# Performance work log

Hardware: AMD Instinct MI355X
Metric: run time of the kernel (lower is better)

Reference implementation:

```python
import jax, jax.numpy as jnp
import numpy as np

N = 10000   # nodes
E = 100000  # edges
B = 64      # graphs
HID = 128


def setup_inputs() -> dict:
    key = jax.random.key(0)
    ks = iter(jax.random.split(key, 64))
    def nrm(shape, s=0.1):
        return jax.random.normal(next(ks), shape, dtype=jnp.float32) * s
    inp = {}
    inp["x"] = nrm((N, 1), 1.0)
    inp["node_type"] = jax.random.randint(next(ks), (N,), 0, 2)
    inp["edge_index"] = jax.random.randint(next(ks), (2, E), 0, N)
    inp["edge_attr"] = nrm((E, 1), 1.0)
    inp["batch"] = jnp.sort(jax.random.randint(next(ks), (N,), 0, B))
    inp["vp_w"] = nrm((1, HID)); inp["vp_b"] = nrm((HID,))
    inp["type_emb"] = nrm((2, HID))
    def conv(pre, fin, h, c):
        inp[pre + "_wl"] = nrm((fin, h * c)); inp[pre + "_bl"] = nrm((h * c,))
        inp[pre + "_wr"] = nrm((fin, h * c)); inp[pre + "_br"] = nrm((h * c,))
        inp[pre + "_we"] = nrm((1, h * c));  inp[pre + "_att"] = nrm((h, c))
        inp[pre + "_bias"] = nrm((h * c if pre != "c3" else c,))
    conv("c1", HID, 8, HID)
    conv("c2", HID * 8, 2, HID)
    conv("c3", HID * 2, 1, HID)
    inp["m1_w"] = nrm((HID, HID)); inp["m1_b"] = nrm((HID,))
    inp["ln1_g"] = jnp.ones((HID,), jnp.float32); inp["ln1_b"] = jnp.zeros((HID,), jnp.float32)
    inp["m2_w"] = nrm((HID, HID // 2)); inp["m2_b"] = nrm((HID // 2,))
    inp["ln2_g"] = jnp.ones((HID // 2,), jnp.float32); inp["ln2_b"] = jnp.zeros((HID // 2,), jnp.float32)
    inp["m3_w"] = nrm((HID // 2, 1)); inp["m3_b"] = nrm((1,))
    return inp


def _gatv2(x, src, dst, ea, wl, bl, wr, br, we, att, bias, heads, out_ch, concat):
    """PyG GATv2Conv (eval mode): add self-loops (edge_attr fill='mean' over dst),
    attn = (att * leaky_relu(Wl x_src + Wr x_dst + We e)).sum(-1), segment-softmax
    over destination, scatter-add of alpha * Wl x_src."""
    n = x.shape[0]
    ones = jnp.ones((ea.shape[0], 1), ea.dtype)
    deg = jax.ops.segment_sum(ones, dst, num_segments=n)
    loop_attr = jax.ops.segment_sum(ea, dst, num_segments=n) / jnp.maximum(deg, 1.0)
    ar = jnp.arange(n, dtype=src.dtype)
    src2 = jnp.concatenate([src, ar])
    dst2 = jnp.concatenate([dst, ar])
    ea2 = jnp.concatenate([ea, loop_attr], axis=0)
    xl = (x @ wl + bl).reshape(n, heads, out_ch)   # source transform
    xr = (x @ wr + br).reshape(n, heads, out_ch)   # target transform
    e = (ea2 @ we).reshape(-1, heads, out_ch)      # [E2, H, C]
    msg = xl[src2]                                 # [E2, H, C]
    z = jax.nn.leaky_relu(msg + xr[dst2] + e, 0.2)
    score = jnp.einsum('ehc,hc->eh', z, att)       # [E2, H]
    smax = jax.ops.segment_max(score, dst2, num_segments=n)
    ex = jnp.exp(score - smax[dst2])
    denom = jax.ops.segment_sum(ex, dst2, num_segments=n)
    alpha = ex / denom[dst2]
    out = jax.ops.segment_sum(alpha[:, :, None] * msg, dst2, num_segments=n)
    out = out.reshape(n, heads * out_ch) if concat else out.mean(axis=1)
    return out + bias


def _layernorm(v, g, b):
    mu = v.mean(-1, keepdims=True)
    var = v.var(-1, keepdims=True)
    return (v - mu) / jnp.sqrt(var + 1e-5) * g + b


def reference(x, node_type, edge_index, edge_attr, batch,
              vp_w, vp_b, type_emb,
              c1_wl, c1_bl, c1_wr, c1_br, c1_we, c1_att, c1_bias,
              c2_wl, c2_bl, c2_wr, c2_br, c2_we, c2_att, c2_bias,
              c3_wl, c3_bl, c3_wr, c3_br, c3_we, c3_att, c3_bias,
              m1_w, m1_b, ln1_g, ln1_b, m2_w, m2_b, ln2_g, ln2_b, m3_w, m3_b):
    src, dst = edge_index[0], edge_index[1]
    h = x @ vp_w + vp_b + type_emb[node_type]
    h = jax.nn.leaky_relu(_gatv2(h, src, dst, edge_attr, c1_wl, c1_bl, c1_wr, c1_br, c1_we, c1_att, c1_bias, 8, HID, True), 0.2)
    h = jax.nn.leaky_relu(_gatv2(h, src, dst, edge_attr, c2_wl, c2_bl, c2_wr, c2_br, c2_we, c2_att, c2_bias, 2, HID, True), 0.2)
    h = jax.nn.leaky_relu(_gatv2(h, src, dst, edge_attr, c3_wl, c3_bl, c3_wr, c3_br, c3_we, c3_att, c3_bias, 1, HID, False), 0.2)
    # masked global mean pool over node_type == 0
    w = (node_type == 0).astype(h.dtype)
    sums = jax.ops.segment_sum(h * w[:, None], batch, num_segments=B)
    cnts = jax.ops.segment_sum(w, batch, num_segments=B)
    pooled = sums / jnp.maximum(cnts, 1.0)[:, None]
    h1 = jax.nn.leaky_relu(_layernorm(pooled @ m1_w + m1_b, ln1_g, ln1_b), 0.2)
    h2 = jax.nn.leaky_relu(_layernorm(h1 @ m2_w + m2_b, ln2_g, ln2_b), 0.2)
    return (h2 @ m3_w + m3_b).squeeze(-1)
```

## Files before the change

kernel.cpp:

```cpp
#include <hip/hip_runtime.h>
#include <math.h>

#define NN 10000
#define NE 100000
#define E2 (NE + NN)
#define NBATCH 64

typedef short bf16x8 __attribute__((ext_vector_type(8)));
typedef float f32x4 __attribute__((ext_vector_type(4)));

__device__ __forceinline__ float lrelu(float v){ return v > 0.f ? v : 0.2f*v; }

__device__ __forceinline__ unsigned short f2bf(float x){
  unsigned int u = __float_as_uint(x);
  u += 0x7fffu + ((u >> 16) & 1u);
  return (unsigned short)(u >> 16);
}
__device__ __forceinline__ float bf2f(unsigned short u){
  return __uint_as_float(((unsigned int)u) << 16);
}

__global__ __launch_bounds__(256) void prep_kernel(
    const float* __restrict__ vp_w, const float* __restrict__ vp_b,
    const float* __restrict__ type_emb,
    const float* __restrict__ c1_wl, const float* __restrict__ c1_bl,
    const float* __restrict__ c1_wr, const float* __restrict__ c1_br,
    float* __restrict__ Ul, float* __restrict__ CTl,
    float* __restrict__ Ur, float* __restrict__ CT2,
    const float* __restrict__ c2_wl, const float* __restrict__ c2_wr,
    const float* __restrict__ c3_wl, const float* __restrict__ c3_wr,
    unsigned short* __restrict__ W2lT, unsigned short* __restrict__ W2rT,
    unsigned short* __restrict__ W3lT, unsigned short* __restrict__ W3rT,
    float* __restrict__ zbase, int zero_words)
{
  __shared__ float t[64][65];
  int b = blockIdx.x;
  int tid = threadIdx.x;
  if (b < 144){
    const float* in; unsigned short* out; int K, N, idx;
    if (b < 64)      { in=c2_wl; out=W2lT; K=1024; N=256; idx=b; }
    else if (b <128) { in=c2_wr; out=W2rT; K=1024; N=256; idx=b-64; }
    else if (b <136) { in=c3_wl; out=W3lT; K=256;  N=128; idx=b-128; }
    else             { in=c3_wr; out=W3rT; K=256;  N=128; idx=b-136; }
    int K64 = K >> 6;
    int kx = idx % K64, nx = idx / K64;
    int k0 = kx*64, n0 = nx*64;
    int lr = tid >> 4;
    int lc = (tid & 15) * 4;
#pragma unroll
    for (int i=0;i<4;++i){
      int r = lr + i*16;
      float4 v = *(const float4*)(in + (size_t)(k0+r)*N + n0 + lc);
      t[r][lc+0]=v.x; t[r][lc+1]=v.y; t[r][lc+2]=v.z; t[r][lc+3]=v.w;
    }
    __syncthreads();
    int sr = tid >> 3;
    int sc = (tid & 7) * 8;
#pragma unroll
    for (int i=0;i<2;++i){
      int n = sr + i*32;
      unsigned short tmp[8];
#pragma unroll
      for (int j=0;j<8;++j) tmp[j] = f2bf(t[sc+j][n]);
      unsigned short* op = out + (size_t)(n0+n)*K + k0 + sc;
      *(ushort4*)op       = make_ushort4(tmp[0],tmp[1],tmp[2],tmp[3]);
      *(ushort4*)(op + 4) = make_ushort4(tmp[4],tmp[5],tmp[6],tmp[7]);
    }
  } else if (b < 148){
    int j = (b-144)*256 + tid;
    float ul=0.f, c0l=0.f, c1l=0.f, ur=0.f, c0r=0.f, c1r=0.f;
    for (int k=0; k<128; ++k){
      float a = c1_wl[k*1024 + j], bb = c1_wr[k*1024 + j];
      float vw = vp_w[k], vb = vp_b[k], t0 = type_emb[k], t1 = type_emb[128+k];
      ul += vw*a; ur += vw*bb;
      c0l += (vb+t0)*a; c1l += (vb+t1)*a;
      c0r += (vb+t0)*bb; c1r += (vb+t1)*bb;
    }
    float bl = c1_bl[j], br = c1_br[j];
    Ul[j]=ul; Ur[j]=ur;
    CTl[j]      = c0l + bl;
    CTl[1024+j] = c1l + bl;
    CT2[j]        = (c0l+bl) + (c0r+br);
    CT2[1024+j]   = (c0l+bl) + (c1r+br);
    CT2[2048+j]   = (c1l+bl) + (c0r+br);
    CT2[3072+j]   = (c1l+bl) + (c1r+br);
  } else {
    for (int i = (b-148)*256 + tid; i < zero_words; i += 32*256)
      zbase[i] = 0.f;
  }
}

__global__ void count_kernel(const int* __restrict__ dst, const float* __restrict__ ea,
                             int* __restrict__ deg, float* __restrict__ loop_sum){
  int e = blockIdx.x*256 + threadIdx.x;
  if (e < NE){
    int d = dst[e];
    atomicAdd(&deg[d], 1);
    atomicAdd(&loop_sum[d], ea[e]);
  }
}

__global__ __launch_bounds__(1024) void scan_kernel(const int* __restrict__ deg,
    const float* __restrict__ loop_sum, int* __restrict__ rowptr, float* __restrict__ loop_attr){
  __shared__ int wsum[16];
  __shared__ int carry_s;
  int tid = threadIdx.x;
  int lane = tid & 63, wid = tid >> 6;
  if (tid == 0) carry_s = 0;
  __syncthreads();
  for (int base = 0; base < NN; base += 1024){
    int i = base + tid;
    int v = (i < NN) ? deg[i] : 0;
    int incl = v;
#pragma unroll
    for (int off = 1; off < 64; off <<= 1){
      int t = __shfl_up(incl, off, 64);
      if (lane >= off) incl += t;
    }
    if (lane == 63) wsum[wid] = incl;
    __syncthreads();
    int pre = carry_s;
    for (int w = 0; w < wid; ++w) pre += wsum[w];
    if (i < NN){
      rowptr[i] = pre + incl - v;
      loop_attr[i] = loop_sum[i] / fmaxf((float)v, 1.f);
    }
    __syncthreads();
    if (tid == 0){
      int t = 0;
      for (int w = 0; w < 16; ++w) t += wsum[w];
      carry_s += t;
    }
    __syncthreads();
  }
  if (tid == 0) rowptr[NN] = carry_s;
}

__global__ void fill_kernel(const int* __restrict__ src, const int* __restrict__ dst,
                            const float* __restrict__ ea, const int* __restrict__ rowptr,
                            int* __restrict__ rowctr, int* __restrict__ srcs,
                            int* __restrict__ dsts, float* __restrict__ eav){
  int e = blockIdx.x*256 + threadIdx.x;
  if (e < NE){
    int d = dst[e];
    int p = rowptr[d] + atomicAdd(&rowctr[d], 1);
    srcs[p] = src[e];
    dsts[p] = d;
    eav[p] = ea[e];
  }
}

__global__ __launch_bounds__(256) void conv1_score(
    const int* __restrict__ srcs, const int* __restrict__ dsts, const float* __restrict__ eav,
    const float* __restrict__ loop_attr, const float* __restrict__ x, const int* __restrict__ ntype,
    const float* __restrict__ Ul, const float* __restrict__ Ur, const float* __restrict__ CT2,
    const float* __restrict__ we, const float* __restrict__ att,
    float* __restrict__ scores)
{
  __shared__ float ldsct[4096];
  int tid = threadIdx.x;
  for (int i = tid; i < 1024; i += 256)
    *(float4*)&ldsct[i*4] = *(const float4*)&CT2[i*4];
  int te = tid & 127;
  int sub = tid >> 7;
  int ch0 = te * 8;
  float ul[8], ur[8], wev[8], atv[8];
#pragma unroll
  for (int v=0; v<8; ++v){
    ul[v]=Ul[ch0+v]; ur[v]=Ur[ch0+v]; wev[v]=we[ch0+v]; atv[v]=att[ch0+v];
  }
  __syncthreads();
  for (int j = blockIdx.x*2 + sub; j < E2; j += gridDim.x*2){
    int s, d; float ea;
    if (j < NE){ s = srcs[j]; d = dsts[j]; ea = eav[j]; }
    else       { s = j - NE;  d = s;       ea = loop_attr[s]; }
    float xs = x[s], xn = x[d];
    int tt = ntype[s]*2 + ntype[d];
    const float* cp = &ldsct[tt*1024 + ch0];
    float4 c0 = *(const float4*)cp;
    float4 c1 = *(const float4*)(cp+4);
    float ct[8] = {c0.x,c0.y,c0.z,c0.w,c1.x,c1.y,c1.z,c1.w};
    float p = 0.f;
#pragma unroll
    for (int v=0; v<8; ++v){
      float z = fmaf(xs, ul[v], fmaf(xn, ur[v], fmaf(ea, wev[v], ct[v])));
      p += atv[v]*lrelu(z);
    }
#pragma unroll
    for (int mm=1; mm<16; mm<<=1) p += __shfl_xor(p, mm, 16);
    if ((te & 15) == 0) scores[(size_t)j*8 + (te>>4)] = p;
  }
}

__global__ __launch_bounds__(256) void conv1_agg(
    const int* __restrict__ rowptr, const int* __restrict__ srcs,
    const float* __restrict__ scores, const float* __restrict__ x, const int* __restrict__ ntype,
    const float* __restrict__ Ul, const float* __restrict__ CTl,
    const float* __restrict__ bias, unsigned short* __restrict__ out)
{
  int n = blockIdx.x;
  int tid = threadIdx.x;
  int h = tid >> 5, el = tid & 31;
  int beg = rowptr[n], deg = rowptr[n+1] - beg;
  int cnt = deg + 1;
  float m = -1e30f, l = 0.f, s1 = 0.f, s20 = 0.f;
  for (int i = el; i < cnt; i += 32){
    int pos; int s;
    if (i < deg){ pos = beg + i; s = srcs[pos]; }
    else        { pos = NE + n;  s = n; }
    float p = scores[(size_t)pos*8 + h];
    float xs = x[s];
    float w0 = (ntype[s] == 0) ? 1.f : 0.f;
    float mn = fmaxf(m, p), f = __expf(m-mn), pe = __expf(p-mn);
    l = l*f + pe; s1 = s1*f + pe*xs; s20 = s20*f + pe*w0; m = mn;
  }
#pragma unroll
  for (int off=1; off<32; off<<=1){
    float mb = __shfl_xor(m, off, 32), lb = __shfl_xor(l, off, 32);
    float s1b = __shfl_xor(s1, off, 32), s20b = __shfl_xor(s20, off, 32);
    float mn = fmaxf(m, mb), fa = __expf(m-mn), fb = __expf(mb-mn);
    l = l*fa + lb*fb; s1 = s1*fa + s1b*fb; s20 = s20*fa + s20b*fb; m = mn;
  }
  float inv = 1.f/l;
  s1 *= inv; s20 *= inv;
  float s21 = 1.f - s20;
  int ch0 = tid * 4;
  float4 u  = *(const float4*)(Ul + ch0);
  float4 t0 = *(const float4*)(CTl + ch0);
  float4 t1 = *(const float4*)(CTl + 1024 + ch0);
  float4 bi = *(const float4*)(bias + ch0);
  ushort4 o;
  o.x = f2bf(lrelu(s1*u.x + s20*t0.x + s21*t1.x + bi.x));
  o.y = f2bf(lrelu(s1*u.y + s20*t0.y + s21*t1.y + bi.y));
  o.z = f2bf(lrelu(s1*u.z + s20*t0.z + s21*t1.z + bi.z));
  o.w = f2bf(lrelu(s1*u.w + s20*t0.w + s21*t1.w + bi.w));
  *(ushort4*)(out + (size_t)n*1024 + ch0) = o;
}

template<int H, int THREADS, int VPT, bool ONLY0, bool OUTBF, bool INBF>
__global__ __launch_bounds__(THREADS) void conv_kernel(
    const int* __restrict__ rowptr, const int* __restrict__ srcs, const float* __restrict__ eav,
    const float* __restrict__ loop_attr, const int* __restrict__ ntype,
    const void* __restrict__ Xv, int stride, int xr_off,
    const float* __restrict__ we, const float* __restrict__ att, const float* __restrict__ bias,
    void* __restrict__ out)
{
  const int HC = THREADS*VPT;
  const int TPH = THREADS/H;
  int n = blockIdx.x;
  if (ONLY0 && ntype[n] != 0) return;
  int tid = threadIdx.x;
  int ch0 = tid * VPT;
  const float* Xf = (const float*)Xv;
  const unsigned short* Xb = (const unsigned short*)Xv;
  float wev[VPT], atv[VPT], biv[VPT], xrv[VPT];
#pragma unroll
  for (int v=0; v<VPT; ++v){
    int ch = ch0+v;
    wev[v]=we[ch]; atv[v]=att[ch]; biv[v]=bias[ch];
  }
  if constexpr (INBF){
    ushort4 q = *(const ushort4*)(Xb + (size_t)n*stride + xr_off + ch0);
    xrv[0]=bf2f(q.x); xrv[1]=bf2f(q.y); xrv[2]=bf2f(q.z); xrv[3]=bf2f(q.w);
  } else {
#pragma unroll
    for (int v=0; v<VPT; ++v) xrv[v]=Xf[(size_t)n*stride + xr_off + ch0+v];
  }
  float ms[4], ls[4], A[4][VPT];
#pragma unroll
  for (int k=0; k<4; ++k){
    ms[k] = -INFINITY; ls[k] = 0.f;
#pragma unroll
    for (int v=0; v<VPT; ++v) A[k][v] = 0.f;
  }
  int beg=rowptr[n], end=rowptr[n+1];
  float la = loop_attr[n];
  for (int j=beg; j<=end; j+=4){
    bool val[4]; int sx[4]; float ex[4];
#pragma unroll
    for (int k=0; k<4; ++k){
      int pos = j + k;
      val[k] = pos <= end;
      sx[k] = (!val[k] || pos == end) ? n : srcs[pos];
      ex[k] = !val[k] ? 0.f : (pos == end ? la : eav[pos]);
    }
    float xv[4][VPT];
#pragma unroll
    for (int k=0; k<4; ++k){
      if constexpr (INBF){
        ushort4 q = *(const ushort4*)(Xb + (size_t)sx[k]*stride + ch0);
        xv[k][0]=bf2f(q.x); xv[k][1]=bf2f(q.y); xv[k][2]=bf2f(q.z); xv[k][3]=bf2f(q.w);
      } else if constexpr (VPT == 4){
        float4 q = *(const float4*)(Xf + (size_t)sx[k]*stride + ch0);
        xv[k][0]=q.x; xv[k][1]=q.y; xv[k][2]=q.z; xv[k][3]=q.w;
      } else {
        float2 q = *(const float2*)(Xf + (size_t)sx[k]*stride + ch0);
        xv[k][0]=q.x; xv[k][1]=q.y;
      }
    }
    float p[4];
#pragma unroll
    for (int k=0; k<4; ++k){
      float acc = 0.f;
#pragma unroll
      for (int v=0; v<VPT; ++v)
        acc += atv[v]*lrelu(xv[k][v]+xrv[v]+ex[k]*wev[v]);
      p[k] = acc;
    }
#pragma unroll
    for (int mm=1; mm<TPH; mm<<=1){
#pragma unroll
      for (int k=0; k<4; ++k) p[k] += __shfl_xor(p[k], mm, 64);
    }
#pragma unroll
    for (int k=0; k<4; ++k){
      if (val[k]){
        float mn=fmaxf(ms[k],p[k]), sc=__expf(ms[k]-mn), pe=__expf(p[k]-mn);
        ls[k]=ls[k]*sc+pe; ms[k]=mn;
#pragma unroll
        for (int v=0; v<VPT; ++v) A[k][v]=A[k][v]*sc+pe*xv[k][v];
      }
    }
  }
#pragma unroll
  for (int k=1; k<4; ++k){
    float mn = fmaxf(ms[0], ms[k]);
    float fa = __expf(ms[0]-mn), fb = __expf(ms[k]-mn);
    ls[0] = ls[0]*fa + ls[k]*fb;
#pragma unroll
    for (int v=0; v<VPT; ++v) A[0][v] = A[0][v]*fa + A[k][v]*fb;
    ms[0] = mn;
  }
  float inv = 1.f/ls[0];
  size_t baseo=(size_t)n*HC+ch0;
  if constexpr (OUTBF){
    unsigned short* ob = (unsigned short*)out;
    ushort4 o;
    o.x = f2bf(lrelu(A[0][0]*inv+biv[0]));
    o.y = f2bf(lrelu(A[0][1]*inv+biv[1]));
    o.z = f2bf(lrelu(A[0][2]*inv+biv[2]));
    o.w = f2bf(lrelu(A[0][3]*inv+biv[3]));
    *(ushort4*)(ob + baseo) = o;
  } else {
    float* of = (float*)out;
#pragma unroll
    for (int v=0; v<VPT; ++v) of[baseo+v]=lrelu(A[0][v]*inv+biv[v]);
  }
}

template<bool OUTBF>
__global__ __launch_bounds__(256) void gemm_dual_lds(
    const short* __restrict__ Abf,
    const short* __restrict__ WlT, const short* __restrict__ WrT,
    const float* __restrict__ bl, const float* __restrict__ br,
    void* __restrict__ Out, int M, int K, int NcH, int cgrid, int rgrid)
{
  __shared__ short lds[12288];
  int id = blockIdx.x;
  int xcd = id & 7, slot = id >> 3;
  int nb = slot % cgrid;
  int rowgroup = (slot / cgrid) * 8 + xcd;
  if (rowgroup >= rgrid) return;
  int row0 = rowgroup * 128;
  int NC2 = 2*NcH;
  int halfx = NcH >> 6;
  int isR = nb >= halfx;
  const short* WT = isR ? WrT : WlT;
  const float* bias = isR ? br : bl;
  int col0 = (nb - (isR ? halfx : 0)) * 64;
  int gcol0 = nb * 64;
  int tid = threadIdx.x;
  int lane = tid & 63, wave = tid >> 6;
  int wm = wave >> 1, wn = wave & 1;
  int quad = lane >> 4, l16 = lane & 15;

  const short* asrc[4];
#pragma unroll
  for (int i=0;i<4;++i){
    int c = wave*256 + i*64 + lane;
    int m = c >> 3, j = c & 7;
    int gr = row0 + m; gr = gr < M ? gr : M-1;
    asrc[i] = Abf + (size_t)gr*K + ((j ^ (m & 7)) << 3);
  }
  const short* bsrc[2];
#pragma unroll
  for (int i=0;i<2;++i){
    int c = wave*128 + i*64 + lane;
    int nloc = c >> 3, j = c & 7;
    bsrc[i] = WT + (size_t)(col0 + nloc)*K + ((j ^ (nloc & 7)) << 3);
  }

  float biasv[2] = { bias[col0 + wn*32 + l16], bias[col0 + wn*32 + 16 + l16] };
  f32x4 acc[4][2];
#pragma unroll
  for (int f=0; f<4; ++f)
#pragma unroll
    for (int g=0; g<2; ++g) acc[f][g] = (f32x4){0.f,0.f,0.f,0.f};

  int niter = K >> 6;
  for (int it=0; it<niter; ++it){
    int k0 = it << 6;
#pragma unroll
    for (int i=0;i<4;++i)
      __builtin_amdgcn_global_load_lds(asrc[i] + k0, &lds[(wave*256 + i*64)*8], 16, 0, 0);
#pragma unroll
    for (int i=0;i<2;++i)
      __builtin_amdgcn_global_load_lds(bsrc[i] + k0, &lds[8192 + (wave*128 + i*64)*8], 16, 0, 0);
    __syncthreads();
#pragma unroll
    for (int s=0; s<2; ++s){
      int t = s*4 + quad;
      bf16x8 af[4], bfv[2];
#pragma unroll
      for (int f=0; f<4; ++f){
        int m = wm*64 + f*16 + l16;
        af[f] = *(const bf16x8*)&lds[m*64 + ((t ^ (m & 7)) << 3)];
      }
#pragma unroll
      for (int g=0; g<2; ++g){
        int nloc = wn*32 + g*16 + l16;
        bfv[g] = *(const bf16x8*)&lds[8192 + nloc*64 + ((t ^ (nloc & 7)) << 3)];
      }
#pragma unroll
      for (int f=0; f<4; ++f)
#pragma unroll
        for (int g=0; g<2; ++g)
          acc[f][g] = __builtin_amdgcn_mfma_f32_16x16x32_bf16(af[f], bfv[g], acc[f][g], 0,0,0);
    }
    __syncthreads();
  }

#pragma unroll
  for (int f=0; f<4; ++f){
    int rbase = row0 + wm*64 + f*16 + quad*4;
#pragma unroll
    for (int r=0; r<4; ++r){
      int rr = rbase + r;
      if (rr < M){
#pragma unroll
        for (int g=0; g<2; ++g){
          int cc = gcol0 + wn*32 + g*16 + l16;
          float val = acc[f][g][r] + biasv[g];
          if constexpr (OUTBF) ((unsigned short*)Out)[(size_t)rr*NC2 + cc] = f2bf(val);
          else                 ((float*)Out)[(size_t)rr*NC2 + cc] = val;
        }
      }
    }
  }
}

__device__ __forceinline__ int lbound(const int* __restrict__ a, int n, int key){
  int lo = 0, hi = n;
  while (lo < hi){ int mid = (lo+hi) >> 1; if (a[mid] < key) lo = mid+1; else hi = mid; }
  return lo;
}

__global__ __launch_bounds__(128) void head_kernel(
    const float* __restrict__ h3, const int* __restrict__ ntype, const int* __restrict__ batch,
    const float* __restrict__ m1w, const float* __restrict__ m1b,
    const float* __restrict__ g1, const float* __restrict__ b1,
    const float* __restrict__ m2w, const float* __restrict__ m2b,
    const float* __restrict__ g2, const float* __restrict__ b2,
    const float* __restrict__ m3w, const float* __restrict__ m3b,
    float* __restrict__ out)
{
  __shared__ float p[128];
  __shared__ float hb[128];
  __shared__ float red[128];
  int b = blockIdx.x, j = threadIdx.x;
  int lo = lbound(batch, NN, b);
  int hi = lbound(batch, NN, b+1);
  float s = 0.f, cnt = 0.f;
  int n = lo;
  for (; n + 3 < hi; n += 4){
    float w0 = (ntype[n]   == 0) ? 1.f : 0.f;
    float w1 = (ntype[n+1] == 0) ? 1.f : 0.f;
    float w2 = (ntype[n+2] == 0) ? 1.f : 0.f;
    float w3 = (ntype[n+3] == 0) ? 1.f : 0.f;
    s += w0*h3[(size_t)n*128 + j]     + w1*h3[(size_t)(n+1)*128 + j]
       + w2*h3[(size_t)(n+2)*128 + j] + w3*h3[(size_t)(n+3)*128 + j];
    cnt += w0 + w1 + w2 + w3;
  }
  for (; n < hi; ++n){
    float w = (ntype[n] == 0) ? 1.f : 0.f;
    s += w*h3[(size_t)n*128 + j];
    cnt += w;
  }
  p[j] = s / fmaxf(cnt, 1.f);
  __syncthreads();
  float a = m1b[j];
  for (int k=0; k<128; ++k) a += p[k]*m1w[k*128 + j];
  red[j] = a; __syncthreads();
  for (int off=64; off>0; off>>=1){ if (j<off) red[j] += red[j+off]; __syncthreads(); }
  float mu = red[0] * (1.f/128.f);
  __syncthreads();
  float d = a - mu;
  red[j] = d*d; __syncthreads();
  for (int off=64; off>0; off>>=1){ if (j<off) red[j] += red[j+off]; __syncthreads(); }
  float var = red[0] * (1.f/128.f);
  __syncthreads();
  hb[j] = lrelu(d * rsqrtf(var + 1e-5f) * g1[j] + b1[j]);
  __syncthreads();
  float a2 = 0.f;
  if (j < 64){
    a2 = m2b[j];
    for (int k=0; k<128; ++k) a2 += hb[k]*m2w[k*64 + j];
  }
  red[j] = (j<64) ? a2 : 0.f; __syncthreads();
  for (int off=64; off>0; off>>=1){ if (j<off) red[j] += red[j+off]; __syncthreads(); }
  float mu2 = red[0] * (1.f/64.f);
  __syncthreads();
  float d2 = a2 - mu2;
  red[j] = (j<64) ? d2*d2 : 0.f; __syncthreads();
  for (int off=64; off>0; off>>=1){ if (j<off) red[j] += red[j+off]; __syncthreads(); }
  float var2 = red[0] * (1.f/64.f);
  __syncthreads();
  if (j < 64) hb[j] = lrelu(d2 * rsqrtf(var2 + 1e-5f) * g2[j] + b2[j]);
  __syncthreads();
  if (j == 0){
    float o = m3b[0];
    for (int k=0; k<64; ++k) o += hb[k]*m3w[k];
    out[b] = o;
  }
}

extern "C" void kernel_launch(void* const* d_in, const int* in_sizes, int n_in,
                              void* d_out, int out_size, void* d_ws, size_t ws_size,
                              hipStream_t stream)
{
  const float* x        = (const float*)d_in[0];
  const int*   ntype    = (const int*)d_in[1];
  const int*   ei       = (const int*)d_in[2];
  const float* eattr    = (const float*)d_in[3];
  const int*   batch    = (const int*)d_in[4];
  const float* vp_w     = (const float*)d_in[5];
  const float* vp_b     = (const float*)d_in[6];
  const float* type_emb = (const float*)d_in[7];
  const float* c1_wl = (const float*)d_in[8];  const float* c1_bl = (const float*)d_in[9];
  const float* c1_wr = (const float*)d_in[10]; const float* c1_br = (const float*)d_in[11];
  const float* c1_we = (const float*)d_in[12]; const float* c1_att= (const float*)d_in[13];
  const float* c1_bias=(const float*)d_in[14];
  const float* c2_wl = (const float*)d_in[15]; const float* c2_bl = (const float*)d_in[16];
  const float* c2_wr = (const float*)d_in[17]; const float* c2_br = (const float*)d_in[18];
  const float* c2_we = (const float*)d_in[19]; const float* c2_att= (const float*)d_in[20];
  const float* c2_bias=(const float*)d_in[21];
  const float* c3_wl = (const float*)d_in[22]; const float* c3_bl = (const float*)d_in[23];
  const float* c3_wr = (const float*)d_in[24]; const float* c3_br = (const float*)d_in[25];
  const float* c3_we = (const float*)d_in[26]; const float* c3_att= (const float*)d_in[27];
  const float* c3_bias=(const float*)d_in[28];
  const float* m1_w = (const float*)d_in[29]; const float* m1_b = (const float*)d_in[30];
  const float* ln1_g= (const float*)d_in[31]; const float* ln1_b= (const float*)d_in[32];
  const float* m2_w = (const float*)d_in[33]; const float* m2_b = (const float*)d_in[34];
  const float* ln2_g= (const float*)d_in[35]; const float* ln2_b= (const float*)d_in[36];
  const float* m3_w = (const float*)d_in[37]; const float* m3_b = (const float*)d_in[38];
  const int* esrc = ei;
  const int* edst = ei + NE;
  float* outp = (float*)d_out;
  (void)in_sizes; (void)n_in; (void)out_size; (void)ws_size;

  char* w = (char*)d_ws;
  auto alloc = [&](size_t bytes) -> void* {
    void* p = (void*)w;
    w += (bytes + 255) & ~(size_t)255;
    return p;
  };
  unsigned short* h1bf = (unsigned short*)alloc((size_t)NN*1024*2);
  unsigned short* X2   = (unsigned short*)alloc((size_t)NN*512*2);
  unsigned short* h2bf = (unsigned short*)alloc((size_t)NN*256*2);
  float* X3   = (float*)alloc((size_t)NN*256*4);
  float* h3   = (float*)alloc((size_t)NN*128*4);
  unsigned short* W2lT = (unsigned short*)alloc((size_t)256*1024*2);
  unsigned short* W2rT = (unsigned short*)alloc((size_t)256*1024*2);
  unsigned short* W3lT = (unsigned short*)alloc((size_t)128*256*2);
  unsigned short* W3rT = (unsigned short*)alloc((size_t)128*256*2);
  float* Ul   = (float*)alloc(1024*4);
  float* CTl  = (float*)alloc(2048*4);
  float* Ur   = (float*)alloc(1024*4);
  float* CT2  = (float*)alloc(4096*4);
  float* scores = (float*)alloc((size_t)E2*8*4);
  const int zero_words = 3*NN;
  float* zbase = (float*)alloc((size_t)zero_words*4);
  int*   deg      = (int*)zbase;
  int*   rowctr   = (int*)(zbase + NN);
  float* loop_sum = zbase + 2*NN;
  float* loop_attr= (float*)alloc((size_t)NN*4);
  int*   rowptr   = (int*)alloc((size_t)(NN+1)*4);
  int*   srcs     = (int*)alloc((size_t)NE*4);
  int*   dsts     = (int*)alloc((size_t)NE*4);
  float* eav      = (float*)alloc((size_t)NE*4);

  prep_kernel<<<180, 256, 0, stream>>>(vp_w, vp_b, type_emb,
      c1_wl, c1_bl, c1_wr, c1_br, Ul, CTl, Ur, CT2,
      c2_wl, c2_wr, c3_wl, c3_wr, W2lT, W2rT, W3lT, W3rT,
      zbase, zero_words);
  count_kernel<<<(NE+255)/256, 256, 0, stream>>>(edst, eattr, deg, loop_sum);
  scan_kernel<<<1, 1024, 0, stream>>>(deg, loop_sum, rowptr, loop_attr);
  fill_kernel<<<(NE+255)/256, 256, 0, stream>>>(esrc, edst, eattr, rowptr, rowctr,
                                                srcs, dsts, eav);
  conv1_score<<<2048, 256, 0, stream>>>(srcs, dsts, eav, loop_attr, x, ntype,
      Ul, Ur, CT2, c1_we, c1_att, scores);
  conv1_agg<<<NN, 256, 0, stream>>>(rowptr, srcs, scores, x, ntype,
      Ul, CTl, c1_bias, h1bf);
  gemm_dual_lds<true><<<640, 256, 0, stream>>>(
      (const short*)h1bf, (const short*)W2lT, (const short*)W2rT, c2_bl, c2_br,
      (void*)X2, NN, 1024, 256, 8, 79);
  conv_kernel<2,64,4,false,true,true><<<NN, 64, 0, stream>>>(rowptr, srcs, eav, loop_attr, ntype,
      (const void*)X2, 512, 256, c2_we, c2_att, c2_bias, h2bf);
  gemm_dual_lds<false><<<320, 256, 0, stream>>>(
      (const short*)h2bf, (const short*)W3lT, (const short*)W3rT, c3_bl, c3_br,
      (void*)X3, NN, 256, 128, 4, 79);
  conv_kernel<1,64,2,true,false,false><<<NN, 64, 0, stream>>>(rowptr, srcs, eav, loop_attr, ntype,
      (const void*)X3, 256, 128, c3_we, c3_att, c3_bias, h3);
  head_kernel<<<NBATCH, 128, 0, stream>>>(h3, ntype, batch, m1_w, m1_b, ln1_g, ln1_b,
                                          m2_w, m2_b, ln2_g, ln2_b, m3_w, m3_b, outp);
}
```

Before: 315.4 us.

## Prefetch next edge in conv1_score, swizzle LDS table, append self-loops to edge arrays

conv1_score now software-pipelines its grid-stride loop, loading the next edge's indices, features and type ahead of computing the current one. The per-type channel table in LDS is XOR-swizzled to cut bank conflicts on the float4 reads. Self-loop entries are written into the extended srcs/dsts/eav arrays during the scan, which removes the branch in the score loop. leaky_relu becomes a branchless fmax form and the accumulation uses fma. The cost is extra registers for the prefetched values and a few more stores in the single-block scan.

New measurement: 318.0 us. About the same (+0.8%).

```diff
diff --git a/kernel.cpp b/kernel.cpp
--- a/kernel.cpp
+++ b/kernel.cpp
@@ -9,7 +9,7 @@
 typedef short bf16x8 __attribute__((ext_vector_type(8)));
 typedef float f32x4 __attribute__((ext_vector_type(4)));
 
-__device__ __forceinline__ float lrelu(float v){ return v > 0.f ? v : 0.2f*v; }
+__device__ __forceinline__ float lrelu(float v){ return fmaxf(v, 0.2f*v); }
 
 __device__ __forceinline__ unsigned short f2bf(float x){
   unsigned int u = __float_as_uint(x);
@@ -101,7 +101,8 @@
 }
 
 __global__ __launch_bounds__(1024) void scan_kernel(const int* __restrict__ deg,
-    const float* __restrict__ loop_sum, int* __restrict__ rowptr, float* __restrict__ loop_attr){
+    const float* __restrict__ loop_sum, int* __restrict__ rowptr, float* __restrict__ loop_attr,
+    int* __restrict__ srcs, int* __restrict__ dsts, float* __restrict__ eav){
   __shared__ int wsum[16];
   __shared__ int carry_s;
   int tid = threadIdx.x;
@@ -123,7 +124,11 @@
     for (int w = 0; w < wid; ++w) pre += wsum[w];
     if (i < NN){
       rowptr[i] = pre + incl - v;
-      loop_attr[i] = loop_sum[i] / fmaxf((float)v, 1.f);
+      float la = loop_sum[i] / fmaxf((float)v, 1.f);
+      loop_attr[i] = la;
+      srcs[NE + i] = i;
+      dsts[NE + i] = i;
+      eav[NE + i]  = la;
     }
     __syncthreads();
     if (tid == 0){
@@ -152,43 +157,59 @@
 
 __global__ __launch_bounds__(256) void conv1_score(
     const int* __restrict__ srcs, const int* __restrict__ dsts, const float* __restrict__ eav,
-    const float* __restrict__ loop_attr, const float* __restrict__ x, const int* __restrict__ ntype,
+    const float* __restrict__ x, const int* __restrict__ ntype,
     const float* __restrict__ Ul, const float* __restrict__ Ur, const float* __restrict__ CT2,
     const float* __restrict__ we, const float* __restrict__ att,
     float* __restrict__ scores)
 {
   __shared__ float ldsct[4096];
   int tid = threadIdx.x;
-  for (int i = tid; i < 1024; i += 256)
-    *(float4*)&ldsct[i*4] = *(const float4*)&CT2[i*4];
+  for (int i = tid; i < 1024; i += 256){
+    int ph = i ^ ((i >> 3) & 7);
+    *(float4*)&ldsct[ph*4] = *(const float4*)&CT2[i*4];
+  }
   int te = tid & 127;
   int sub = tid >> 7;
   int ch0 = te * 8;
+  int m = (te >> 2) & 7;
+  int roff0 = ((2*te)     ^ m) << 2;
+  int roff1 = ((2*te + 1) ^ m) << 2;
   float ul[8], ur[8], wev[8], atv[8];
 #pragma unroll
   for (int v=0; v<8; ++v){
     ul[v]=Ul[ch0+v]; ur[v]=Ur[ch0+v]; wev[v]=we[ch0+v]; atv[v]=att[ch0+v];
   }
   __syncthreads();
-  for (int j = blockIdx.x*2 + sub; j < E2; j += gridDim.x*2){
-    int s, d; float ea;
-    if (j < NE){ s = srcs[j]; d = dsts[j]; ea = eav[j]; }
-    else       { s = j - NE;  d = s;       ea = loop_attr[s]; }
-    float xs = x[s], xn = x[d];
-    int tt = ntype[s]*2 + ntype[d];
-    const float* cp = &ldsct[tt*1024 + ch0];
-    float4 c0 = *(const float4*)cp;
-    float4 c1 = *(const float4*)(cp+4);
+  const int stride = gridDim.x*2;
+  int j = blockIdx.x*2 + sub;
+  if (j >= E2) return;
+  int s = srcs[j], d = dsts[j];
+  float ea = eav[j];
+  float xs = x[s], xn = x[d];
+  int tt = ntype[s]*2 + ntype[d];
+  while (true){
+    int jn = j + stride;
+    bool hn = jn < E2;
+    int s2 = 0, d2 = 0; float ea2 = 0.f;
+    if (hn){ s2 = srcs[jn]; d2 = dsts[jn]; ea2 = eav[jn]; }
+    float xs2 = 0.f, xn2 = 0.f; int tt2 = 0;
+    if (hn){ xs2 = x[s2]; xn2 = x[d2]; tt2 = ntype[s2]*2 + ntype[d2]; }
+    const float* rowp = &ldsct[tt*1024];
+    float4 c0 = *(const float4*)(rowp + roff0);
+    float4 c1 = *(const float4*)(rowp + roff1);
     float ct[8] = {c0.x,c0.y,c0.z,c0.w,c1.x,c1.y,c1.z,c1.w};
     float p = 0.f;
 #pragma unroll
     for (int v=0; v<8; ++v){
       float z = fmaf(xs, ul[v], fmaf(xn, ur[v], fmaf(ea, wev[v], ct[v])));
-      p += atv[v]*lrelu(z);
+      float zl = fmaxf(z, 0.2f*z);
+      p = fmaf(atv[v], zl, p);
     }
 #pragma unroll
     for (int mm=1; mm<16; mm<<=1) p += __shfl_xor(p, mm, 16);
     if ((te & 15) == 0) scores[(size_t)j*8 + (te>>4)] = p;
+    if (!hn) break;
+    j = jn; s = s2; d = d2; ea = ea2; xs = xs2; xn = xn2; tt = tt2;
   }
 }
 
@@ -585,19 +606,19 @@
   float* loop_sum = zbase + 2*NN;
   float* loop_attr= (float*)alloc((size_t)NN*4);
   int*   rowptr   = (int*)alloc((size_t)(NN+1)*4);
-  int*   srcs     = (int*)alloc((size_t)NE*4);
-  int*   dsts     = (int*)alloc((size_t)NE*4);
-  float* eav      = (float*)alloc((size_t)NE*4);
+  int*   srcs     = (int*)alloc((size_t)E2*4);
+  int*   dsts     = (int*)alloc((size_t)E2*4);
+  float* eav      = (float*)alloc((size_t)E2*4);
 
   prep_kernel<<<180, 256, 0, stream>>>(vp_w, vp_b, type_emb,
       c1_wl, c1_bl, c1_wr, c1_br, Ul, CTl, Ur, CT2,
       c2_wl, c2_wr, c3_wl, c3_wr, W2lT, W2rT, W3lT, W3rT,
       zbase, zero_words);
   count_kernel<<<(NE+255)/256, 256, 0, stream>>>(edst, eattr, deg, loop_sum);
-  scan_kernel<<<1, 1024, 0, stream>>>(deg, loop_sum, rowptr, loop_attr);
+  scan_kernel<<<1, 1024, 0, stream>>>(deg, loop_sum, rowptr, loop_attr, srcs, dsts, eav);
   fill_kernel<<<(NE+255)/256, 256, 0, stream>>>(esrc, edst, eattr, rowptr, rowctr,
                                                 srcs, dsts, eav);
-  conv1_score<<<2048, 256, 0, stream>>>(srcs, dsts, eav, loop_attr, x, ntype,
+  conv1_score<<<2048, 256, 0, stream>>>(srcs, dsts, eav, x, ntype,
       Ul, Ur, CT2, c1_we, c1_att, scores);
   conv1_agg<<<NN, 256, 0, stream>>>(rowptr, srcs, scores, x, ntype,
       Ul, CTl, c1_bias, h1bf);
```

## Fuse conv1 score and aggregation into one per-node kernel; pack nodes per block

Applied to the files above, without the earlier changes.

Replaces the separate edge-score kernel, which wrote an E2x8 score buffer, and the per-node aggregation kernel with a single kernel. Each 128-thread group handles one destination node, computes attention scores on the fly with prefetch of the next edge, and runs the online softmax. This removes the scores round trip and the dsts array. The conv2/conv3 kernels now pack 4 nodes per 256-thread block instead of one node per 64-thread block, and lrelu becomes fmaxf. The trade-off is that the fused conv1 walks each node's edges serially inside one group, which may lengthen latency chains for high-degree nodes.

Result: no change. 316.1 us (+0.2%).

```diff
diff --git a/kernel.cpp b/kernel.cpp
--- a/kernel.cpp
+++ b/kernel.cpp
@@ -9,7 +9,7 @@
 typedef short bf16x8 __attribute__((ext_vector_type(8)));
 typedef float f32x4 __attribute__((ext_vector_type(4)));
 
-__device__ __forceinline__ float lrelu(float v){ return v > 0.f ? v : 0.2f*v; }
+__device__ __forceinline__ float lrelu(float v){ return fmaxf(v, 0.2f*v); }
 
 __device__ __forceinline__ unsigned short f2bf(float x){
   unsigned int u = __float_as_uint(x);
@@ -26,7 +26,7 @@
     const float* __restrict__ c1_wl, const float* __restrict__ c1_bl,
     const float* __restrict__ c1_wr, const float* __restrict__ c1_br,
     float* __restrict__ Ul, float* __restrict__ CTl,
-    float* __restrict__ Ur, float* __restrict__ CT2,
+    float* __restrict__ Ur, float* __restrict__ CTr,
     const float* __restrict__ c2_wl, const float* __restrict__ c2_wr,
     const float* __restrict__ c3_wl, const float* __restrict__ c3_wr,
     unsigned short* __restrict__ W2lT, unsigned short* __restrict__ W2rT,
@@ -80,10 +80,8 @@
     Ul[j]=ul; Ur[j]=ur;
     CTl[j]      = c0l + bl;
     CTl[1024+j] = c1l + bl;
-    CT2[j]        = (c0l+bl) + (c0r+br);
-    CT2[1024+j]   = (c0l+bl) + (c1r+br);
-    CT2[2048+j]   = (c1l+bl) + (c0r+br);
-    CT2[3072+j]   = (c1l+bl) + (c1r+br);
+    CTr[j]      = c0r + br;
+    CTr[1024+j] = c1r + br;
   } else {
     for (int i = (b-148)*256 + tid; i < zero_words; i += 32*256)
       zbase[i] = 0.f;
@@ -139,117 +137,94 @@
 __global__ void fill_kernel(const int* __restrict__ src, const int* __restrict__ dst,
                             const float* __restrict__ ea, const int* __restrict__ rowptr,
                             int* __restrict__ rowctr, int* __restrict__ srcs,
-                            int* __restrict__ dsts, float* __restrict__ eav){
+                            float* __restrict__ eav){
   int e = blockIdx.x*256 + threadIdx.x;
   if (e < NE){
     int d = dst[e];
     int p = rowptr[d] + atomicAdd(&rowctr[d], 1);
     srcs[p] = src[e];
-    dsts[p] = d;
     eav[p] = ea[e];
   }
 }
 
-__global__ __launch_bounds__(256) void conv1_score(
-    const int* __restrict__ srcs, const int* __restrict__ dsts, const float* __restrict__ eav,
-    const float* __restrict__ loop_attr, const float* __restrict__ x, const int* __restrict__ ntype,
-    const float* __restrict__ Ul, const float* __restrict__ Ur, const float* __restrict__ CT2,
+__global__ __launch_bounds__(256) void conv1_fused(
+    const int* __restrict__ rowptr, const int* __restrict__ srcs,
+    const float* __restrict__ eav, const float* __restrict__ loop_attr,
+    const float* __restrict__ x, const int* __restrict__ ntype,
+    const float* __restrict__ Ul, const float* __restrict__ Ur,
+    const float* __restrict__ CTl, const float* __restrict__ CTr,
     const float* __restrict__ we, const float* __restrict__ att,
-    float* __restrict__ scores)
-{
-  __shared__ float ldsct[4096];
-  int tid = threadIdx.x;
-  for (int i = tid; i < 1024; i += 256)
-    *(float4*)&ldsct[i*4] = *(const float4*)&CT2[i*4];
-  int te = tid & 127;
-  int sub = tid >> 7;
-  int ch0 = te * 8;
-  float ul[8], ur[8], wev[8], atv[8];
-#pragma unroll
-  for (int v=0; v<8; ++v){
-    ul[v]=Ul[ch0+v]; ur[v]=Ur[ch0+v]; wev[v]=we[ch0+v]; atv[v]=att[ch0+v];
-  }
-  __syncthreads();
-  for (int j = blockIdx.x*2 + sub; j < E2; j += gridDim.x*2){
-    int s, d; float ea;
-    if (j < NE){ s = srcs[j]; d = dsts[j]; ea = eav[j]; }
-    else       { s = j - NE;  d = s;       ea = loop_attr[s]; }
-    float xs = x[s], xn = x[d];
-    int tt = ntype[s]*2 + ntype[d];
-    const float* cp = &ldsct[tt*1024 + ch0];
-    float4 c0 = *(const float4*)cp;
-    float4 c1 = *(const float4*)(cp+4);
-    float ct[8] = {c0.x,c0.y,c0.z,c0.w,c1.x,c1.y,c1.z,c1.w};
-    float p = 0.f;
-#pragma unroll
-    for (int v=0; v<8; ++v){
-      float z = fmaf(xs, ul[v], fmaf(xn, ur[v], fmaf(ea, wev[v], ct[v])));
-      p += atv[v]*lrelu(z);
-    }
-#pragma unroll
-    for (int mm=1; mm<16; mm<<=1) p += __shfl_xor(p, mm, 16);
-    if ((te & 15) == 0) scores[(size_t)j*8 + (te>>4)] = p;
-  }
-}
-
-__global__ __launch_bounds__(256) void conv1_agg(
-    const int* __restrict__ rowptr, const int* __restrict__ srcs,
-    const float* __restrict__ scores, const float* __restrict__ x, const int* __restrict__ ntype,
-    const float* __restrict__ Ul, const float* __restrict__ CTl,
     const float* __restrict__ bias, unsigned short* __restrict__ out)
 {
-  int n = blockIdx.x;
-  int tid = threadIdx.x;
-  int h = tid >> 5, el = tid & 31;
-  int beg = rowptr[n], deg = rowptr[n+1] - beg;
-  int cnt = deg + 1;
+  int n = blockIdx.x*2 + (threadIdx.x >> 7);
+  if (n >= NN) return;
+  int te = threadIdx.x & 127;
+  int ch0 = te * 8;
+  float ul[8], we8[8], atv[8], ctl0[8], ctl1[8], cn[8];
+#pragma unroll
+  for (int v=0; v<8; ++v){
+    ul[v]=Ul[ch0+v]; we8[v]=we[ch0+v]; atv[v]=att[ch0+v];
+    ctl0[v]=CTl[ch0+v]; ctl1[v]=CTl[1024+ch0+v];
+  }
+  int beg = rowptr[n], deg = rowptr[n+1]-beg;
+  float xn = x[n]; int tn = ntype[n]; float la = loop_attr[n];
+  {
+    const float* ctr = tn ? (CTr+1024) : CTr;
+#pragma unroll
+    for (int v=0; v<8; ++v) cn[v] = fmaf(xn, Ur[ch0+v], ctr[ch0+v]);
+  }
   float m = -1e30f, l = 0.f, s1 = 0.f, s20 = 0.f;
-  for (int i = el; i < cnt; i += 32){
-    int pos; int s;
-    if (i < deg){ pos = beg + i; s = srcs[pos]; }
-    else        { pos = NE + n;  s = n; }
-    float p = scores[(size_t)pos*8 + h];
-    float xs = x[s];
-    float w0 = (ntype[s] == 0) ? 1.f : 0.f;
-    float mn = fmaxf(m, p), f = __expf(m-mn), pe = __expf(p-mn);
-    l = l*f + pe; s1 = s1*f + pe*xs; s20 = s20*f + pe*w0; m = mn;
-  }
-#pragma unroll
-  for (int off=1; off<32; off<<=1){
-    float mb = __shfl_xor(m, off, 32), lb = __shfl_xor(l, off, 32);
-    float s1b = __shfl_xor(s1, off, 32), s20b = __shfl_xor(s20, off, 32);
-    float mn = fmaxf(m, mb), fa = __expf(m-mn), fb = __expf(mb-mn);
-    l = l*fa + lb*fb; s1 = s1*fa + s1b*fb; s20 = s20*fa + s20b*fb; m = mn;
+  int   sc = (deg>0) ? srcs[beg] : n;
+  float ec = (deg>0) ? eav[beg]  : la;
+  float xsc = x[sc]; int tsc = ntype[sc];
+  for (int idx=0; idx<=deg; ++idx){
+    int nx = idx+1;
+    int sn2; float en2;
+    if (nx < deg){ sn2 = srcs[beg+nx]; en2 = eav[beg+nx]; }
+    else         { sn2 = n;            en2 = la; }
+    float xsn = x[sn2]; int tsn = ntype[sn2];
+    float acc = 0.f;
+#pragma unroll
+    for (int v=0; v<8; ++v){
+      float t = cn[v] + (tsc ? ctl1[v] : ctl0[v]);
+      float z = fmaf(xsc, ul[v], fmaf(ec, we8[v], t));
+      acc = fmaf(atv[v], fmaxf(z, 0.2f*z), acc);
+    }
+#pragma unroll
+    for (int mm=1; mm<16; mm<<=1) acc += __shfl_xor(acc, mm, 16);
+    float w0 = (tsc == 0) ? 1.f : 0.f;
+    float mn = fmaxf(m, acc), f = __expf(m-mn), pe = __expf(acc-mn);
+    l = l*f + pe; s1 = s1*f + pe*xsc; s20 = s20*f + pe*w0; m = mn;
+    sc = sn2; ec = en2; xsc = xsn; tsc = tsn;
   }
   float inv = 1.f/l;
   s1 *= inv; s20 *= inv;
   float s21 = 1.f - s20;
-  int ch0 = tid * 4;
-  float4 u  = *(const float4*)(Ul + ch0);
-  float4 t0 = *(const float4*)(CTl + ch0);
-  float4 t1 = *(const float4*)(CTl + 1024 + ch0);
-  float4 bi = *(const float4*)(bias + ch0);
-  ushort4 o;
-  o.x = f2bf(lrelu(s1*u.x + s20*t0.x + s21*t1.x + bi.x));
-  o.y = f2bf(lrelu(s1*u.y + s20*t0.y + s21*t1.y + bi.y));
-  o.z = f2bf(lrelu(s1*u.z + s20*t0.z + s21*t1.z + bi.z));
-  o.w = f2bf(lrelu(s1*u.w + s20*t0.w + s21*t1.w + bi.w));
-  *(ushort4*)(out + (size_t)n*1024 + ch0) = o;
-}
-
-template<int H, int THREADS, int VPT, bool ONLY0, bool OUTBF, bool INBF>
-__global__ __launch_bounds__(THREADS) void conv_kernel(
+  float4 bi0 = *(const float4*)(bias + ch0);
+  float4 bi1 = *(const float4*)(bias + ch0 + 4);
+  float bv[8] = {bi0.x,bi0.y,bi0.z,bi0.w,bi1.x,bi1.y,bi1.z,bi1.w};
+  unsigned short o[8];
+#pragma unroll
+  for (int v=0; v<8; ++v)
+    o[v] = f2bf(lrelu(s1*ul[v] + s20*ctl0[v] + s21*ctl1[v] + bv[v]));
+  *(ushort4*)(out + (size_t)n*1024 + ch0)     = make_ushort4(o[0],o[1],o[2],o[3]);
+  *(ushort4*)(out + (size_t)n*1024 + ch0 + 4) = make_ushort4(o[4],o[5],o[6],o[7]);
+}
+
+template<int H, int NPB, int VPT, bool ONLY0, bool OUTBF, bool INBF>
+__global__ __launch_bounds__(64*NPB) void conv_kernel(
     const int* __restrict__ rowptr, const int* __restrict__ srcs, const float* __restrict__ eav,
     const float* __restrict__ loop_attr, const int* __restrict__ ntype,
     const void* __restrict__ Xv, int stride, int xr_off,
     const float* __restrict__ we, const float* __restrict__ att, const float* __restrict__ bias,
     void* __restrict__ out)
 {
-  const int HC = THREADS*VPT;
-  const int TPH = THREADS/H;
-  int n = blockIdx.x;
+  const int HC = 64*VPT;
+  const int TPH = 64/H;
+  int n = blockIdx.x*NPB + (threadIdx.x >> 6);
+  if (n >= NN) return;
   if (ONLY0 && ntype[n] != 0) return;
-  int tid = threadIdx.x;
+  int tid = threadIdx.x & 63;
   int ch0 = tid * VPT;
   const float* Xf = (const float*)Xv;
   const unsigned short* Xb = (const unsigned short*)Xv;
@@ -576,8 +551,7 @@
   float* Ul   = (float*)alloc(1024*4);
   float* CTl  = (float*)alloc(2048*4);
   float* Ur   = (float*)alloc(1024*4);
-  float* CT2  = (float*)alloc(4096*4);
-  float* scores = (float*)alloc((size_t)E2*8*4);
+  float* CTr  = (float*)alloc(2048*4);
   const int zero_words = 3*NN;
   float* zbase = (float*)alloc((size_t)zero_words*4);
   int*   deg      = (int*)zbase;
@@ -586,30 +560,27 @@
   float* loop_attr= (float*)alloc((size_t)NN*4);
   int*   rowptr   = (int*)alloc((size_t)(NN+1)*4);
   int*   srcs     = (int*)alloc((size_t)NE*4);
-  int*   dsts     = (int*)alloc((size_t)NE*4);
   float* eav      = (float*)alloc((size_t)NE*4);
 
   prep_kernel<<<180, 256, 0, stream>>>(vp_w, vp_b, type_emb,
-      c1_wl, c1_bl, c1_wr, c1_br, Ul, CTl, Ur, CT2,
+      c1_wl, c1_bl, c1_wr, c1_br, Ul, CTl, Ur, CTr,
       c2_wl, c2_wr, c3_wl, c3_wr, W2lT, W2rT, W3lT, W3rT,
       zbase, zero_words);
   count_kernel<<<(NE+255)/256, 256, 0, stream>>>(edst, eattr, deg, loop_sum);
   scan_kernel<<<1, 1024, 0, stream>>>(deg, loop_sum, rowptr, loop_attr);
   fill_kernel<<<(NE+255)/256, 256, 0, stream>>>(esrc, edst, eattr, rowptr, rowctr,
-                                                srcs, dsts, eav);
-  conv1_score<<<2048, 256, 0, stream>>>(srcs, dsts, eav, loop_attr, x, ntype,
-      Ul, Ur, CT2, c1_we, c1_att, scores);
-  conv1_agg<<<NN, 256, 0, stream>>>(rowptr, srcs, scores, x, ntype,
-      Ul, CTl, c1_bias, h1bf);
+                                                srcs, eav);
+  conv1_fused<<<NN/2, 256, 0, stream>>>(rowptr, srcs, eav, loop_attr, x, ntype,
+      Ul, Ur, CTl, CTr, c1_we, c1_att, c1_bias, h1bf);
   gemm_dual_lds<true><<<640, 256, 0, stream>>>(
       (const short*)h1bf, (const short*)W2lT, (const short*)W2rT, c2_bl, c2_br,
       (void*)X2, NN, 1024, 256, 8, 79);
-  conv_kernel<2,64,4,false,true,true><<<NN, 64, 0, stream>>>(rowptr, srcs, eav, loop_attr, ntype,
+  conv_kernel<2,4,4,false,true,true><<<NN/4, 256, 0, stream>>>(rowptr, srcs, eav, loop_attr, ntype,
       (const void*)X2, 512, 256, c2_we, c2_att, c2_bias, h2bf);
   gemm_dual_lds<false><<<320, 256, 0, stream>>>(
       (const short*)h2bf, (const short*)W3lT, (const short*)W3rT, c3_bl, c3_br,
       (void*)X3, NN, 256, 128, 4, 79);
-  conv_kernel<1,64,2,true,false,false><<<NN, 64, 0, stream>>>(rowptr, srcs, eav, loop_attr, ntype,
+  conv_kernel<1,4,2,true,false,false><<<NN/4, 256, 0, stream>>>(rowptr, srcs, eav, loop_attr, ntype,
       (const void*)X3, 256, 128, c3_we, c3_att, c3_bias, h3);
   head_kernel<<<NBATCH, 128, 0, stream>>>(h3, ntype, batch, m1_w, m1_b, ln1_g, ln1_b,
                                           m2_w, m2_b, ln2_g, ln2_b, m3_w, m3_b, outp);
```
